# Optimization experiments

Measured on AMD Instinct MI355X. Metric: run time of the kernel, lower is better.

## Reference

```python
import jax, jax.numpy as jnp
import numpy as np

IN_FEATURES = 8192
OUT_FEATURES = 8192
WEIGHT_PER_OUT = 32
BATCH = 1024


def setup_inputs() -> dict:
    key = jax.random.key(0)
    k1, k2, k3 = jax.random.split(key, 3)
    x = jax.random.normal(k1, (BATCH, IN_FEATURES), dtype=jnp.float32)
    connections = jax.random.randint(k2, (OUT_FEATURES, WEIGHT_PER_OUT), 0, IN_FEATURES, dtype=jnp.int32)
    bound = 1.0 / np.sqrt(WEIGHT_PER_OUT)
    weights = jax.random.uniform(k3, (OUT_FEATURES, WEIGHT_PER_OUT), dtype=jnp.float32, minval=-bound, maxval=bound)
    return {"x": x, "connections": connections, "weights": weights}


def reference(x, connections, weights):
    # x: [B, In]; connections, weights: [O, K]
    # out[b, o] = sum_k x[b, connections[o, k]] * weights[o, k]
    gathered = jnp.take(x, connections, axis=1)  # [B, O, K]
    return jnp.einsum('bok,ok->bo', gathered, weights)
```

## Files before the change

### kernel.cpp

```cpp
#include <hip/hip_runtime.h>
#include <hip/hip_fp16.h>


constexpr int IN_F    = 8192;
constexpr int OUT_F   = 8192;
constexpr int KPER    = 32;
constexpr int BATCH   = 1024;
constexpr int ROWS    = 4;
constexpr int THREADS = 512;
constexpr int OHALF   = OUT_F / 2;
constexpr size_t PK_BYTES = (size_t)OUT_F * (KPER / 2) * 16;

__global__ __launch_bounds__(256)
void psl_repack(const int* __restrict__ conn, const float* __restrict__ w,
                uint4* __restrict__ pk) {
    const int t  = blockIdx.x * 256 + threadIdx.x;
    const int o  = t >> 4;
    const int k2 = t & 15;
    const int base = o * KPER + k2 * 2;
    uint4 v;
    v.x = (unsigned)conn[base];
    v.y = __float_as_uint(w[base]);
    v.z = (unsigned)conn[base + 1];
    v.w = __float_as_uint(w[base + 1]);
    pk[(size_t)k2 * OUT_F + o] = v;
}

__global__ __launch_bounds__(THREADS, 4)
void psl_main(const float* __restrict__ x, const uint4* __restrict__ pk,
              float* __restrict__ out) {
    __shared__ uint2 lds_x[IN_F];

    const int tid = threadIdx.x;
    const int bt  = blockIdx.x >> 1;
    const int oh  = blockIdx.x & 1;
    const long b0 = (long)bt * ROWS;

    const float* xr0 = x + (b0 + 0) * IN_F;
    const float* xr1 = x + (b0 + 1) * IN_F;
    const float* xr2 = x + (b0 + 2) * IN_F;
    const float* xr3 = x + (b0 + 3) * IN_F;

    for (int c = tid; c < IN_F; c += THREADS) {
        __half2 h01 = __floats2half2_rn(xr0[c], xr1[c]);
        __half2 h23 = __floats2half2_rn(xr2[c], xr3[c]);
        uint2 pkx;
        pkx.x = *reinterpret_cast<unsigned*>(&h01);
        pkx.y = *reinterpret_cast<unsigned*>(&h23);
        lds_x[c] = pkx;
    }
    __syncthreads();

    float* or0 = out + (b0 + 0) * OUT_F;
    float* or1 = out + (b0 + 1) * OUT_F;
    float* or2 = out + (b0 + 2) * OUT_F;
    float* or3 = out + (b0 + 3) * OUT_F;

    const int obase = oh * OHALF;

    for (int j = 0; j < OHALF / THREADS; ++j) {
        const int o = obase + j * THREADS + tid;
        float a0 = 0.f, a1 = 0.f, a2 = 0.f, a3 = 0.f;

#pragma unroll
        for (int k2 = 0; k2 < KPER / 2; ++k2) {
            const uint4 v = pk[(size_t)k2 * OUT_F + o];
            const uint2 g0 = lds_x[v.x];
            const uint2 g1 = lds_x[v.z];
            const float w0 = __uint_as_float(v.y);
            const float w1 = __uint_as_float(v.w);

            __half2 h01 = *reinterpret_cast<const __half2*>(&g0.x);
            __half2 h23 = *reinterpret_cast<const __half2*>(&g0.y);
            float2 f01 = __half22float2(h01);
            float2 f23 = __half22float2(h23);
            a0 = fmaf(f01.x, w0, a0);
            a1 = fmaf(f01.y, w0, a1);
            a2 = fmaf(f23.x, w0, a2);
            a3 = fmaf(f23.y, w0, a3);

            h01 = *reinterpret_cast<const __half2*>(&g1.x);
            h23 = *reinterpret_cast<const __half2*>(&g1.y);
            f01 = __half22float2(h01);
            f23 = __half22float2(h23);
            a0 = fmaf(f01.x, w1, a0);
            a1 = fmaf(f01.y, w1, a1);
            a2 = fmaf(f23.x, w1, a2);
            a3 = fmaf(f23.y, w1, a3);
        }

        or0[o] = a0;
        or1[o] = a1;
        or2[o] = a2;
        or3[o] = a3;
    }
}

__global__ __launch_bounds__(THREADS, 4)
void psl_fallback(const float* __restrict__ x, const int* __restrict__ conn,
                  const float* __restrict__ w, float* __restrict__ out) {
    __shared__ uint2 lds_x[IN_F];
    const int tid = threadIdx.x;
    const int bt  = blockIdx.x >> 1;
    const int oh  = blockIdx.x & 1;
    const long b0 = (long)bt * ROWS;
    const float* xr0 = x + (b0 + 0) * IN_F;
    const float* xr1 = x + (b0 + 1) * IN_F;
    const float* xr2 = x + (b0 + 2) * IN_F;
    const float* xr3 = x + (b0 + 3) * IN_F;
    for (int c = tid; c < IN_F; c += THREADS) {
        __half2 h01 = __floats2half2_rn(xr0[c], xr1[c]);
        __half2 h23 = __floats2half2_rn(xr2[c], xr3[c]);
        uint2 pkx;
        pkx.x = *reinterpret_cast<unsigned*>(&h01);
        pkx.y = *reinterpret_cast<unsigned*>(&h23);
        lds_x[c] = pkx;
    }
    __syncthreads();
    float* or0 = out + (b0 + 0) * OUT_F;
    float* or1 = out + (b0 + 1) * OUT_F;
    float* or2 = out + (b0 + 2) * OUT_F;
    float* or3 = out + (b0 + 3) * OUT_F;
    const int obase = oh * OHALF;
    for (int j = 0; j < OHALF / THREADS; ++j) {
        const int o = obase + j * THREADS + tid;
        const int4*   c4 = reinterpret_cast<const int4*>(conn + (size_t)o * KPER);
        const float4* w4 = reinterpret_cast<const float4*>(w + (size_t)o * KPER);
        float a0 = 0.f, a1 = 0.f, a2 = 0.f, a3 = 0.f;
#define GACC(IDX, WT)                                              \
        {                                                          \
            uint2 v = lds_x[(IDX)];                                \
            __half2 h01 = *reinterpret_cast<__half2*>(&v.x);       \
            __half2 h23 = *reinterpret_cast<__half2*>(&v.y);       \
            float2 f01 = __half22float2(h01);                      \
            float2 f23 = __half22float2(h23);                      \
            a0 = fmaf(f01.x, (WT), a0);                            \
            a1 = fmaf(f01.y, (WT), a1);                            \
            a2 = fmaf(f23.x, (WT), a2);                            \
            a3 = fmaf(f23.y, (WT), a3);                            \
        }
#pragma unroll
        for (int jj = 0; jj < KPER / 4; ++jj) {
            const int4   ci = c4[jj];
            const float4 wj = w4[jj];
            GACC(ci.x, wj.x);
            GACC(ci.y, wj.y);
            GACC(ci.z, wj.z);
            GACC(ci.w, wj.w);
        }
#undef GACC
        or0[o] = a0;
        or1[o] = a1;
        or2[o] = a2;
        or3[o] = a3;
    }
}

extern "C" void kernel_launch(void* const* d_in, const int* in_sizes, int n_in,
                              void* d_out, int out_size, void* d_ws, size_t ws_size,
                              hipStream_t stream) {
    const float* x    = (const float*)d_in[0];
    const int*   conn = (const int*)d_in[1];
    const float* w    = (const float*)d_in[2];
    float*       out  = (float*)d_out;

    if (ws_size >= PK_BYTES) {
        uint4* pk = (uint4*)d_ws;
        psl_repack<<<dim3(OUT_F * (KPER / 2) / 256), 256, 0, stream>>>(conn, w, pk);
        psl_main<<<dim3((BATCH / ROWS) * 2), THREADS, 0, stream>>>(x, pk, out);
    } else {
        psl_fallback<<<dim3((BATCH / ROWS) * 2), THREADS, 0, stream>>>(x, conn, w, out);
    }
}
```

Measured before the change: 117.1 us.

## Pack fp16 weights with byte offsets and use fdot2 accumulation

The repack now stores four connections per 16-byte record, as 16-bit byte offsets into LDS plus fp16 weight pairs. This halves the packed-stream traffic and drops the index-to-address multiply. The main loop gathers four LDS entries, byte-permutes them into row pairs and accumulates with v_dot2 fp16 instructions instead of converting to fp32 and doing separate FMAs. The block size doubles to 1024 threads. Weights are rounded to fp16, which loses precision, and the 64KB LDS per block limits occupancy.

New measurement: 104.2 us. 1.12x faster.

```diff
diff --git a/kernel.cpp b/kernel.cpp
--- a/kernel.cpp
+++ b/kernel.cpp
@@ -1,32 +1,47 @@
 #include <hip/hip_runtime.h>
 #include <hip/hip_fp16.h>
 
+
+typedef _Float16 half2_t __attribute__((ext_vector_type(2)));
 
 constexpr int IN_F    = 8192;
 constexpr int OUT_F   = 8192;
 constexpr int KPER    = 32;
 constexpr int BATCH   = 1024;
 constexpr int ROWS    = 4;
-constexpr int THREADS = 512;
+constexpr int THREADS = 1024;
 constexpr int OHALF   = OUT_F / 2;
-constexpr size_t PK_BYTES = (size_t)OUT_F * (KPER / 2) * 16;
+constexpr size_t PK_BYTES = (size_t)OUT_F * (KPER / 4) * 16;
 
 __global__ __launch_bounds__(256)
 void psl_repack(const int* __restrict__ conn, const float* __restrict__ w,
                 uint4* __restrict__ pk) {
-    const int t  = blockIdx.x * 256 + threadIdx.x;
-    const int o  = t >> 4;
-    const int k2 = t & 15;
-    const int base = o * KPER + k2 * 2;
+    const int t = blockIdx.x * 256 + threadIdx.x;
+    const int j = t >> 13;
+    const int o = t & (OUT_F - 1);
+    const int base = o * KPER + j * 4;
+    const int4   ci = *reinterpret_cast<const int4*>(conn + base);
+    const float4 wj = *reinterpret_cast<const float4*>(w + base);
     uint4 v;
-    v.x = (unsigned)conn[base];
-    v.y = __float_as_uint(w[base]);
-    v.z = (unsigned)conn[base + 1];
-    v.w = __float_as_uint(w[base + 1]);
-    pk[(size_t)k2 * OUT_F + o] = v;
+    v.x = ((unsigned)ci.x << 3) | ((unsigned)ci.y << 19);
+    v.z = ((unsigned)ci.z << 3) | ((unsigned)ci.w << 19);
+    __half2 w01 = __floats2half2_rn(wj.x, wj.y);
+    __half2 w23 = __floats2half2_rn(wj.z, wj.w);
+    v.y = *reinterpret_cast<unsigned*>(&w01);
+    v.w = *reinterpret_cast<unsigned*>(&w23);
+    pk[(size_t)j * OUT_F + o] = v;
 }
 
-__global__ __launch_bounds__(THREADS, 4)
+__device__ __forceinline__ float dot2acc(unsigned hi, unsigned lo,
+                                         unsigned sel, unsigned wbits,
+                                         float acc) {
+    unsigned p = __builtin_amdgcn_perm(hi, lo, sel);
+    return __builtin_amdgcn_fdot2(__builtin_bit_cast(half2_t, p),
+                                  __builtin_bit_cast(half2_t, wbits),
+                                  acc, false);
+}
+
+__global__ __launch_bounds__(THREADS, 8)
 void psl_main(const float* __restrict__ x, const uint4* __restrict__ pk,
               float* __restrict__ out) {
     __shared__ uint2 lds_x[IN_F];
@@ -57,36 +72,31 @@
     float* or3 = out + (b0 + 3) * OUT_F;
 
     const int obase = oh * OHALF;
+    const char* ldsb = reinterpret_cast<const char*>(lds_x);
 
-    for (int j = 0; j < OHALF / THREADS; ++j) {
-        const int o = obase + j * THREADS + tid;
+    for (int jj = 0; jj < OHALF / THREADS; ++jj) {
+        const int o = obase + jj * THREADS + tid;
+        const uint4* pkrow = pk + o;
+
         float a0 = 0.f, a1 = 0.f, a2 = 0.f, a3 = 0.f;
 
-#pragma unroll
-        for (int k2 = 0; k2 < KPER / 2; ++k2) {
-            const uint4 v = pk[(size_t)k2 * OUT_F + o];
-            const uint2 g0 = lds_x[v.x];
-            const uint2 g1 = lds_x[v.z];
-            const float w0 = __uint_as_float(v.y);
-            const float w1 = __uint_as_float(v.w);
-
-            __half2 h01 = *reinterpret_cast<const __half2*>(&g0.x);
-            __half2 h23 = *reinterpret_cast<const __half2*>(&g0.y);
-            float2 f01 = __half22float2(h01);
-            float2 f23 = __half22float2(h23);
-            a0 = fmaf(f01.x, w0, a0);
-            a1 = fmaf(f01.y, w0, a1);
-            a2 = fmaf(f23.x, w0, a2);
-            a3 = fmaf(f23.y, w0, a3);
-
-            h01 = *reinterpret_cast<const __half2*>(&g1.x);
-            h23 = *reinterpret_cast<const __half2*>(&g1.y);
-            f01 = __half22float2(h01);
-            f23 = __half22float2(h23);
-            a0 = fmaf(f01.x, w1, a0);
-            a1 = fmaf(f01.y, w1, a1);
-            a2 = fmaf(f23.x, w1, a2);
-            a3 = fmaf(f23.y, w1, a3);
+#pragma unroll 2
+        for (int j = 0; j < KPER / 4; ++j) {
+            const uint4 v = pkrow[(size_t)j * OUT_F];
+            const unsigned off0 = v.x & 0xFFFFu, off1 = v.x >> 16;
+            const unsigned off2 = v.z & 0xFFFFu, off3 = v.z >> 16;
+            const uint2 g0 = *reinterpret_cast<const uint2*>(ldsb + off0);
+            const uint2 g1 = *reinterpret_cast<const uint2*>(ldsb + off1);
+            const uint2 g2 = *reinterpret_cast<const uint2*>(ldsb + off2);
+            const uint2 g3 = *reinterpret_cast<const uint2*>(ldsb + off3);
+            a0 = dot2acc(g1.x, g0.x, 0x05040100u, v.y, a0);
+            a1 = dot2acc(g1.x, g0.x, 0x07060302u, v.y, a1);
+            a2 = dot2acc(g1.y, g0.y, 0x05040100u, v.y, a2);
+            a3 = dot2acc(g1.y, g0.y, 0x07060302u, v.y, a3);
+            a0 = dot2acc(g3.x, g2.x, 0x05040100u, v.w, a0);
+            a1 = dot2acc(g3.x, g2.x, 0x07060302u, v.w, a1);
+            a2 = dot2acc(g3.y, g2.y, 0x05040100u, v.w, a2);
+            a3 = dot2acc(g3.y, g2.y, 0x07060302u, v.w, a3);
         }
 
         or0[o] = a0;
@@ -96,7 +106,7 @@
     }
 }
 
-__global__ __launch_bounds__(THREADS, 4)
+__global__ __launch_bounds__(512, 4)
 void psl_fallback(const float* __restrict__ x, const int* __restrict__ conn,
                   const float* __restrict__ w, float* __restrict__ out) {
     __shared__ uint2 lds_x[IN_F];
@@ -108,7 +118,7 @@
     const float* xr1 = x + (b0 + 1) * IN_F;
     const float* xr2 = x + (b0 + 2) * IN_F;
     const float* xr3 = x + (b0 + 3) * IN_F;
-    for (int c = tid; c < IN_F; c += THREADS) {
+    for (int c = tid; c < IN_F; c += 512) {
         __half2 h01 = __floats2half2_rn(xr0[c], xr1[c]);
         __half2 h23 = __floats2half2_rn(xr2[c], xr3[c]);
         uint2 pkx;
@@ -122,8 +132,8 @@
     float* or2 = out + (b0 + 2) * OUT_F;
     float* or3 = out + (b0 + 3) * OUT_F;
     const int obase = oh * OHALF;
-    for (int j = 0; j < OHALF / THREADS; ++j) {
-        const int o = obase + j * THREADS + tid;
+    for (int j = 0; j < OHALF / 512; ++j) {
+        const int o = obase + j * 512 + tid;
         const int4*   c4 = reinterpret_cast<const int4*>(conn + (size_t)o * KPER);
         const float4* w4 = reinterpret_cast<const float4*>(w + (size_t)o * KPER);
         float a0 = 0.f, a1 = 0.f, a2 = 0.f, a3 = 0.f;
@@ -166,9 +176,9 @@
 
     if (ws_size >= PK_BYTES) {
         uint4* pk = (uint4*)d_ws;
-        psl_repack<<<dim3(OUT_F * (KPER / 2) / 256), 256, 0, stream>>>(conn, w, pk);
+        psl_repack<<<dim3(OUT_F * (KPER / 4) / 256), 256, 0, stream>>>(conn, w, pk);
         psl_main<<<dim3((BATCH / ROWS) * 2), THREADS, 0, stream>>>(x, pk, out);
     } else {
-        psl_fallback<<<dim3((BATCH / ROWS) * 2), THREADS, 0, stream>>>(x, conn, w, out);
+        psl_fallback<<<dim3((BATCH / ROWS) * 2), 512, 0, stream>>>(x, conn, w, out);
     }
 }
```
